# Kernel tuning notes

Hardware: AMD Instinct MI355X
Metric: run time of the kernel (lower is better)

## Reference

```python
import jax, jax.numpy as jnp
import numpy as np

MIN_RANGE, MAX_RANGE = 0, 2
N, Z, Y, X = 2, 40, 400, 400   # voxel map dims
G = 30000                       # number of grid query positions
M = 120000                      # number of points (feature rows)
C = 64                          # feature channels


def _build_index_offset():
    # replicates TorchGrouper.__init__
    r = np.concatenate([np.arange(-MAX_RANGE, -MIN_RANGE), np.arange(MIN_RANGE, MAX_RANGE)])
    p = r.shape[0]
    rx = np.broadcast_to(r.reshape(1, 1, -1), (p, p, p))
    ry = np.broadcast_to(r.reshape(1, -1, 1), (p, p, p))
    rz = np.broadcast_to(r.reshape(-1, 1, 1), (p, p, p))
    off = np.stack([np.zeros_like(rx), rx, ry, rz], axis=3).reshape(1, -1, 4)
    return jnp.asarray(off, dtype=jnp.int32)  # [1, K, 4]


def setup_inputs() -> dict:
    key = jax.random.key(0)
    k1, k2, k3, k4, k5 = jax.random.split(key, 5)
    # voxel map entries: -1 = empty voxel, else point index in [0, M)
    voxel_maps = jax.random.randint(k1, (N, Z, Y, X), -1, M, dtype=jnp.int32)
    grid_positions = jnp.stack([
        jax.random.randint(k2, (G,), 0, N),
        jax.random.randint(k3, (G,), 0, Z),
        jax.random.randint(k4, (G,), 0, Y),
        jax.random.randint(k5, (G,), 0, X),
    ], axis=1).astype(jnp.int32)  # [G, 4]
    features = jax.random.normal(jax.random.fold_in(key, 7), (M, C), dtype=jnp.float32)
    return {
        "voxel_maps": voxel_maps,
        "grid_positions": grid_positions,
        "features": features,
        "index_offset": _build_index_offset(),
    }


def reference(voxel_maps, grid_positions, features, index_offset):
    Nn, Zz, Yy, Xx = voxel_maps.shape
    Gn = grid_positions.shape[0]
    K = index_offset.shape[1]
    Cc = features.shape[1]

    # broadcast offsets onto every grid position: [G, K, 4]
    pos = grid_positions[:, None, :].astype(jnp.int32) + index_offset
    n = pos[..., 0]
    z = jnp.clip(pos[..., 1], 0, Zz - 1)
    y = jnp.clip(pos[..., 2], 0, Yy - 1)
    x = jnp.clip(pos[..., 3], 0, Xx - 1)

    # voxel lookup -> point indices, -1 means empty  [G, K]
    sampled_idx = voxel_maps[n, z, y, x]

    # prepend zero-feature row so index -1 maps to zeros
    feat = jnp.concatenate([jnp.zeros((1, Cc), features.dtype), features], axis=0)  # [M+1, C]
    sf = feat[sampled_idx + 1]                         # [G, K, C]
    sampled_features = jnp.transpose(sf, (2, 0, 1))[None]  # [1, C, G, K]

    # position feature: clamped integer positions lose fractional part (floor diff = 0),
    # then the raw integer offsets are added back, matching the original math.
    pos_clamped = jnp.stack([n, z, y, x], axis=-1)     # [G, K, 4]
    gpf = jnp.transpose(pos_clamped, (2, 0, 1))[None].astype(features.dtype)  # [1, 4, G, K]
    gpf = gpf - jnp.floor(gpf)
    gpf = gpf + jnp.transpose(index_offset[0]).astype(features.dtype)[None, :, None, :]

    empty_mask = (sampled_idx + 1).sum(axis=1) == 0    # [G]
    return sampled_features, gpf, empty_mask
```

## Files before the change

kernel.cpp:

```cpp
#include <hip/hip_runtime.h>

constexpr int N_ = 2, Z_ = 40, Y_ = 400, X_ = 400;
constexpr int G_ = 30000;
constexpr int M_ = 120000;
constexpr int C_ = 64;
constexpr int K_ = 64;

constexpr int LSTR = C_ + 1;


__global__ __launch_bounds__(256) void grouper_kernel(
    const int*   __restrict__ voxel_maps,
    const int*   __restrict__ grid_positions,
    const float* __restrict__ features,
    const int*   __restrict__ index_offset,
    float*       __restrict__ out)
{
    __shared__ int   s_idx[K_];
    __shared__ float s_feat[C_ * LSTR];

    const int g = blockIdx.x;
    const int t = threadIdx.x;

    const long long GK = (long long)G_ * K_;
    float* out_sf   = out;
    float* out_gpf  = out + (long long)C_ * GK;
    float* out_mask = out + (long long)(C_ + 4) * GK;

    if (t < K_) {
        const int k = t;
        const int4 off = ((const int4*)index_offset)[k];
        const int4 gp  = ((const int4*)grid_positions)[g];

        const int n = gp.x + off.x;
        const int z = min(max(gp.y + off.y, 0), Z_ - 1);
        const int y = min(max(gp.z + off.z, 0), Y_ - 1);
        const int x = min(max(gp.w + off.w, 0), X_ - 1);

        const int sidx = voxel_maps[((n * Z_ + z) * Y_ + y) * X_ + x];
        s_idx[k] = sidx;

        const bool all_empty = __all(sidx == -1);
        if (k == 0) out_mask[g] = all_empty ? 1.0f : 0.0f;
    } else if (t < 2 * K_) {
        const int k = t - K_;
        const int4 off = ((const int4*)index_offset)[k];
        const long long gk = (long long)g * K_ + k;
        out_gpf[0 * GK + gk] = (float)off.x;
        out_gpf[1 * GK + gk] = (float)off.y;
        out_gpf[2 * GK + gk] = (float)off.z;
        out_gpf[3 * GK + gk] = (float)off.w;
    }
    __syncthreads();

    {
        const int q  = t & 15;
        const int kr = t >> 4;
        #pragma unroll
        for (int p = 0; p < 4; ++p) {
            const int k    = p * 16 + kr;
            const int sidx = s_idx[k];
            float4 v = make_float4(0.f, 0.f, 0.f, 0.f);
            if (sidx >= 0)
                v = ((const float4*)(features + (long long)sidx * C_))[q];
            const int c0 = q * 4;
            s_feat[(c0 + 0) * LSTR + k] = v.x;
            s_feat[(c0 + 1) * LSTR + k] = v.y;
            s_feat[(c0 + 2) * LSTR + k] = v.z;
            s_feat[(c0 + 3) * LSTR + k] = v.w;
        }
    }
    __syncthreads();

    {
        const int kq = (t & 15) * 4;
        const int cr = t >> 4;
        const long long base = (long long)g * K_;
        #pragma unroll
        for (int p = 0; p < 4; ++p) {
            const int c = p * 16 + cr;
            float4 v;
            v.x = s_feat[c * LSTR + kq + 0];
            v.y = s_feat[c * LSTR + kq + 1];
            v.z = s_feat[c * LSTR + kq + 2];
            v.w = s_feat[c * LSTR + kq + 3];
            *(float4*)(out_sf + (long long)c * GK + base + kq) = v;
        }
    }
}

extern "C" void kernel_launch(void* const* d_in, const int* in_sizes, int n_in,
                              void* d_out, int out_size, void* d_ws, size_t ws_size,
                              hipStream_t stream) {
    const int*   voxel_maps     = (const int*)d_in[0];
    const int*   grid_positions = (const int*)d_in[1];
    const float* features       = (const float*)d_in[2];
    const int*   index_offset   = (const int*)d_in[3];
    float*       out            = (float*)d_out;

    grouper_kernel<<<G_, 256, 0, stream>>>(
        voxel_maps, grid_positions, features, index_offset, out);
}
```

Baseline: 627.9 us.

## Process eight grid positions per block with channel-group staged transposes

Measured after the change: 660.2 us. +5.1%, slower.

```diff
diff --git a/kernel.cpp b/kernel.cpp
--- a/kernel.cpp
+++ b/kernel.cpp
@@ -6,85 +6,101 @@
 constexpr int C_ = 64;
 constexpr int K_ = 64;
 
-constexpr int LSTR = C_ + 1;
+constexpr int GPB   = 8;
+constexpr int SLOTS = GPB * K_;
+constexpr int CG    = 16;
+constexpr int NGRP  = C_ / CG;
+constexpr int STR   = SLOTS + 4;
 
 
-__global__ __launch_bounds__(256) void grouper_kernel(
+__global__ __launch_bounds__(512) void grouper_kernel(
     const int*   __restrict__ voxel_maps,
     const int*   __restrict__ grid_positions,
     const float* __restrict__ features,
     const int*   __restrict__ index_offset,
     float*       __restrict__ out)
 {
-    __shared__ int   s_idx[K_];
-    __shared__ float s_feat[C_ * LSTR];
+    __shared__ float s_feat[CG * STR];
+    __shared__ int   s_idx[SLOTS];
 
-    const int g = blockIdx.x;
-    const int t = threadIdx.x;
+    constexpr int NWG = G_ / GPB;
+    constexpr int NX  = 8;
+    constexpr int q_  = NWG / NX;
+    constexpr int r_  = NWG % NX;
+    const int bid = blockIdx.x;
+    const int xcd = bid % NX, bi = bid / NX;
+    const int swz = (xcd < r_) ? xcd * (q_ + 1) + bi
+                               : r_ * (q_ + 1) + (xcd - r_) * q_ + bi;
+    const int g0 = swz * GPB;
+
+    const int t    = threadIdx.x;
+    const int lane = t & 63;
+    const int w    = t >> 6;
 
     const long long GK = (long long)G_ * K_;
     float* out_sf   = out;
     float* out_gpf  = out + (long long)C_ * GK;
     float* out_mask = out + (long long)(C_ + 4) * GK;
 
-    if (t < K_) {
-        const int k = t;
-        const int4 off = ((const int4*)index_offset)[k];
-        const int4 gp  = ((const int4*)grid_positions)[g];
+    const int4 off = ((const int4*)index_offset)[lane];
+    const int4 gp  = ((const int4*)grid_positions)[g0 + w];
 
-        const int n = gp.x + off.x;
-        const int z = min(max(gp.y + off.y, 0), Z_ - 1);
-        const int y = min(max(gp.z + off.z, 0), Y_ - 1);
-        const int x = min(max(gp.w + off.w, 0), X_ - 1);
+    const int n = gp.x + off.x;
+    const int z = min(max(gp.y + off.y, 0), Z_ - 1);
+    const int y = min(max(gp.z + off.z, 0), Y_ - 1);
+    const int x = min(max(gp.w + off.w, 0), X_ - 1);
 
-        const int sidx = voxel_maps[((n * Z_ + z) * Y_ + y) * X_ + x];
-        s_idx[k] = sidx;
+    const int sidx = voxel_maps[((n * Z_ + z) * Y_ + y) * X_ + x];
+    s_idx[t] = sidx;
 
-        const bool all_empty = __all(sidx == -1);
-        if (k == 0) out_mask[g] = all_empty ? 1.0f : 0.0f;
-    } else if (t < 2 * K_) {
-        const int k = t - K_;
-        const int4 off = ((const int4*)index_offset)[k];
-        const long long gk = (long long)g * K_ + k;
-        out_gpf[0 * GK + gk] = (float)off.x;
-        out_gpf[1 * GK + gk] = (float)off.y;
-        out_gpf[2 * GK + gk] = (float)off.z;
-        out_gpf[3 * GK + gk] = (float)off.w;
-    }
+    const bool all_empty = __all(sidx == -1);
+    if (lane == 0) out_mask[g0 + w] = all_empty ? 1.0f : 0.0f;
+
+    const long long base_gk = (long long)g0 * K_;
+    out_gpf[0 * GK + base_gk + t] = (float)off.x;
+    out_gpf[1 * GK + base_gk + t] = (float)off.y;
+    out_gpf[2 * GK + base_gk + t] = (float)off.z;
+    out_gpf[3 * GK + base_gk + t] = (float)off.w;
+
     __syncthreads();
 
-    {
-        const int q  = t & 15;
-        const int kr = t >> 4;
+    const int rq = t >> 2;
+    const int qc = t & 3;
+
+    for (int grp = 0; grp < NGRP; ++grp) {
+        float4 v[4];
         #pragma unroll
-        for (int p = 0; p < 4; ++p) {
-            const int k    = p * 16 + kr;
-            const int sidx = s_idx[k];
-            float4 v = make_float4(0.f, 0.f, 0.f, 0.f);
-            if (sidx >= 0)
-                v = ((const float4*)(features + (long long)sidx * C_))[q];
-            const int c0 = q * 4;
-            s_feat[(c0 + 0) * LSTR + k] = v.x;
-            s_feat[(c0 + 1) * LSTR + k] = v.y;
-            s_feat[(c0 + 2) * LSTR + k] = v.z;
-            s_feat[(c0 + 3) * LSTR + k] = v.w;
+        for (int s = 0; s < 4; ++s) {
+            const int slot = s * 128 + rq;
+            const int si   = s_idx[slot];
+            float4 vv = make_float4(0.f, 0.f, 0.f, 0.f);
+            if (si >= 0)
+                vv = ((const float4*)(features + (long long)si * C_))[grp * 4 + qc];
+            v[s] = vv;
         }
-    }
-    __syncthreads();
 
-    {
-        const int kq = (t & 15) * 4;
-        const int cr = t >> 4;
-        const long long base = (long long)g * K_;
+        if (grp) __syncthreads();
+
         #pragma unroll
-        for (int p = 0; p < 4; ++p) {
-            const int c = p * 16 + cr;
-            float4 v;
-            v.x = s_feat[c * LSTR + kq + 0];
-            v.y = s_feat[c * LSTR + kq + 1];
-            v.z = s_feat[c * LSTR + kq + 2];
-            v.w = s_feat[c * LSTR + kq + 3];
-            *(float4*)(out_sf + (long long)c * GK + base + kq) = v;
+        for (int s = 0; s < 4; ++s) {
+            const int slot = s * 128 + rq;
+            s_feat[(qc * 4 + 0) * STR + slot] = v[s].x;
+            s_feat[(qc * 4 + 1) * STR + slot] = v[s].y;
+            s_feat[(qc * 4 + 2) * STR + slot] = v[s].z;
+            s_feat[(qc * 4 + 3) * STR + slot] = v[s].w;
+        }
+        __syncthreads();
+
+        #pragma unroll
+        for (int cc = 0; cc < 2; ++cc) {
+            const int cl = w * 2 + cc;
+            const int c  = grp * CG + cl;
+            #pragma unroll
+            for (int h = 0; h < 2; ++h) {
+                const int sq = h * 64 + lane;
+                const float4 vv = *(const float4*)&s_feat[cl * STR + sq * 4];
+                *(float4*)(out_sf + (long long)c * GK + base_gk + sq * 4) = vv;
+            }
         }
     }
 }
@@ -98,6 +114,6 @@
     const int*   index_offset   = (const int*)d_in[3];
     float*       out            = (float*)d_out;
 
-    grouper_kernel<<<G_, 256, 0, stream>>>(
+    grouper_kernel<<<G_ / GPB, 512, 0, stream>>>(
         voxel_maps, grid_positions, features, index_offset, out);
 }
```
